# Kernel optimization log

Hardware: AMD Instinct MI355X
Metric: run time of the kernel (lower is better)

Reference implementation:

```python
import jax, jax.numpy as jnp
import numpy as np

F_TOKENS = 1024
D_TOKEN = 64
HIDDEN = 128


def setup_inputs() -> dict:
    key = jax.random.key(0)
    k1, k2, k3, k4, k5 = jax.random.split(key, 5)
    node = jax.random.normal(k1, (F_TOKENS, D_TOKEN), dtype=jnp.float32)
    # nn.Linear default init scale ~ 1/sqrt(fan_in); keep simple scaled randn
    W1 = jax.random.normal(k2, (2 * D_TOKEN, HIDDEN), dtype=jnp.float32) / np.sqrt(2 * D_TOKEN)
    b1 = jax.random.normal(k3, (HIDDEN,), dtype=jnp.float32) * 0.01
    w2 = jax.random.normal(k4, (HIDDEN,), dtype=jnp.float32) / np.sqrt(HIDDEN)
    b2 = jax.random.normal(k5, (1,), dtype=jnp.float32) * 0.01
    return {"node": node, "W1": W1, "b1": b1, "w2": w2, "b2": b2}


def reference(node, W1, b1, w2, b2):
    # Original: pair[i,j] = concat(node[i], node[j]);
    # Linear(2d->h) on the concat splits exactly into two d->h matmuls,
    # so we avoid materializing the [F,F,2d] concat tensor (same math).
    d = node.shape[1]
    a = node @ W1[:d]          # [F, h] contribution of v_i
    b = node @ W1[d:]          # [F, h] contribution of v_j
    h = jax.nn.gelu(a[:, None, :] + b[None, :, :] + b1, approximate=False)  # [F, F, h]
    logits = h @ w2 + b2[0]    # [F, F]
    return jax.nn.softmax(logits, axis=-1)
```

## Files before the change

kernel.cpp:

```cpp
#include <hip/hip_runtime.h>
#include <math.h>

#define F 1024
#define D 64
#define H 128

typedef float v2f __attribute__((ext_vector_type(2)));

__global__ __launch_bounds__(128) void prep_kernel(
    const float* __restrict__ node, const float* __restrict__ W1,
    const float* __restrict__ b1,
    float* __restrict__ A, float* __restrict__ Bt) {
  const int i = blockIdx.x;
  const int k = threadIdx.x;
  __shared__ float n[D];
  if (k < D) n[k] = node[i * D + k];
  __syncthreads();
  float a = b1[k];
  float b = 0.f;
#pragma unroll
  for (int r = 0; r < D; ++r) {
    const float nv = n[r];
    a = fmaf(nv, W1[r * H + k], a);
    b = fmaf(nv, W1[(D + r) * H + k], b);
  }
  A[i * H + k] = a;
  Bt[k * F + i] = b;
}

#define C1 (-2.3022082f)
#define C2 (-0.10294323f)

__device__ __forceinline__ void gelu_acc_pk(float a, v2f b, float wk, v2f& acc) {
  const v2f X = a + b;
  const v2f U = X * X;
  const v2f P = __builtin_elementwise_fma((v2f)(C2), U, (v2f)(C1));
  const v2f Arg = X * P;
  v2f E;
  E.x = __builtin_amdgcn_exp2f(Arg.x);
  E.y = __builtin_amdgcn_exp2f(Arg.y);
  const v2f Dn = 1.0f + E;
  v2f R;
  R.x = __builtin_amdgcn_rcpf(Dn.x);
  R.y = __builtin_amdgcn_rcpf(Dn.y);
  const v2f WX = wk * X;
  acc = __builtin_elementwise_fma(WX, R, acc);
}

__global__ __launch_bounds__(512) void pair_kernel(
    const float* __restrict__ A, const float* __restrict__ Bt,
    const float* __restrict__ w2, float* __restrict__ out) {
  const int i0 = blockIdx.x * 2;
  const int tid = threadIdx.x;

  __shared__ float4 sAW[H];
  __shared__ float redm[8][2];
  __shared__ float reds[8][2];

  if (tid < H)
    sAW[tid] = make_float4(A[i0 * H + tid], A[(i0 + 1) * H + tid], w2[tid], 0.f);
  __syncthreads();

  v2f acc0 = {0.f, 0.f};
  v2f acc1 = {0.f, 0.f};

  const v2f* bp = reinterpret_cast<const v2f*>(Bt) + tid;
#pragma unroll 8
  for (int k = 0; k < H; ++k) {
    const v2f b = *bp;
    bp += F / 2;
    const float4 aw = sAW[k];
    gelu_acc_pk(aw.x, b, aw.z, acc0);
    gelu_acc_pk(aw.y, b, aw.z, acc1);
  }

  const int wave = tid >> 6;
  const int lane = tid & 63;

  float m0 = fmaxf(acc0.x, acc0.y);
  float m1 = fmaxf(acc1.x, acc1.y);
#pragma unroll
  for (int off = 32; off >= 1; off >>= 1) {
    m0 = fmaxf(m0, __shfl_xor(m0, off, 64));
    m1 = fmaxf(m1, __shfl_xor(m1, off, 64));
  }
  if (lane == 0) {
    redm[wave][0] = m0;
    redm[wave][1] = m1;
  }
  __syncthreads();
  m0 = redm[0][0];
  m1 = redm[0][1];
#pragma unroll
  for (int w = 1; w < 8; ++w) {
    m0 = fmaxf(m0, redm[w][0]);
    m1 = fmaxf(m1, redm[w][1]);
  }

  float e00 = __expf(acc0.x - m0);
  float e01 = __expf(acc0.y - m0);
  float e10 = __expf(acc1.x - m1);
  float e11 = __expf(acc1.y - m1);
  float s0 = e00 + e01;
  float s1 = e10 + e11;
#pragma unroll
  for (int off = 32; off >= 1; off >>= 1) {
    s0 += __shfl_xor(s0, off, 64);
    s1 += __shfl_xor(s1, off, 64);
  }
  if (lane == 0) {
    reds[wave][0] = s0;
    reds[wave][1] = s1;
  }
  __syncthreads();
  s0 = 0.f;
  s1 = 0.f;
#pragma unroll
  for (int w = 0; w < 8; ++w) {
    s0 += reds[w][0];
    s1 += reds[w][1];
  }

  const float inv0 = __builtin_amdgcn_rcpf(s0);
  const float inv1 = __builtin_amdgcn_rcpf(s1);
  float2 o0, o1;
  o0.x = e00 * inv0;
  o0.y = e01 * inv0;
  o1.x = e10 * inv1;
  o1.y = e11 * inv1;
  *reinterpret_cast<float2*>(out + (size_t)i0 * F + 2 * tid) = o0;
  *reinterpret_cast<float2*>(out + (size_t)(i0 + 1) * F + 2 * tid) = o1;
}

extern "C" void kernel_launch(void* const* d_in, const int* in_sizes, int n_in,
                              void* d_out, int out_size, void* d_ws, size_t ws_size,
                              hipStream_t stream) {
  const float* node = (const float*)d_in[0];
  const float* W1   = (const float*)d_in[1];
  const float* b1   = (const float*)d_in[2];
  const float* w2   = (const float*)d_in[3];
  float* out = (float*)d_out;

  float* A  = (float*)d_ws;
  float* Bt = A + (size_t)F * H;

  prep_kernel<<<F, H, 0, stream>>>(node, W1, b1, A, Bt);
  pair_kernel<<<F / 2, 512, 0, stream>>>(A, Bt, w2, out);
}
```

Measured before the change: 44.34 us.

## Double-buffer Bt tiles into LDS via global_load_lds in pair kernel

Instead of each thread loading its Bt column pair directly from global memory on every k iteration, the pair kernel now stages 8-row tiles of Bt into shared memory with async global_load_lds, double-buffered. Compute on one tile overlaps the load of the next. The goal is to hide global-load latency behind the GELU arithmetic. In exchange it uses 64KB of LDS per block, which lowers occupancy, and it adds a barrier per tile. w2 is now read from global memory rather than packed into shared memory.

```diff
diff --git a/kernel.cpp b/kernel.cpp
--- a/kernel.cpp
+++ b/kernel.cpp
@@ -4,6 +4,8 @@
 #define F 1024
 #define D 64
 #define H 128
+#define BK 8
+#define NT (H / BK)
 
 typedef float v2f __attribute__((ext_vector_type(2)));
 
@@ -43,8 +45,7 @@
   v2f R;
   R.x = __builtin_amdgcn_rcpf(Dn.x);
   R.y = __builtin_amdgcn_rcpf(Dn.y);
-  const v2f WX = wk * X;
-  acc = __builtin_elementwise_fma(WX, R, acc);
+  acc = __builtin_elementwise_fma(wk * X, R, acc);
 }
 
 __global__ __launch_bounds__(512) void pair_kernel(
@@ -52,30 +53,61 @@
     const float* __restrict__ w2, float* __restrict__ out) {
   const int i0 = blockIdx.x * 2;
   const int tid = threadIdx.x;
+  const int wave = tid >> 6;
+  const int lane = tid & 63;
 
-  __shared__ float4 sAW[H];
+  __shared__ float bufs[2][BK * F];
+  __shared__ float2 sA[H];
   __shared__ float redm[8][2];
   __shared__ float reds[8][2];
 
   if (tid < H)
-    sAW[tid] = make_float4(A[i0 * H + tid], A[(i0 + 1) * H + tid], w2[tid], 0.f);
+    sA[tid] = make_float2(A[i0 * H + tid], A[(i0 + 1) * H + tid]);
+
+  const char* const bt_base = (const char*)Bt;
+#define STAGE(buf_, tile_)                                                   \
+  {                                                                          \
+    const char* src_ = bt_base + (size_t)(tile_) * (BK * F * 4);             \
+    _Pragma("unroll")                                                        \
+    for (int r_ = 0; r_ < 4; ++r_) {                                         \
+      const int chunk_ = r_ * 8192 + wave * 1024;                            \
+      __builtin_amdgcn_global_load_lds(                                      \
+          (const __attribute__((address_space(1))) void*)(src_ + chunk_ +    \
+                                                          lane * 16),        \
+          (__attribute__((address_space(3))) void*)((char*)&bufs[buf_][0] +  \
+                                                    chunk_),                 \
+          16, 0, 0);                                                         \
+    }                                                                        \
+  }
+
+  STAGE(0, 0);
   __syncthreads();
 
   v2f acc0 = {0.f, 0.f};
   v2f acc1 = {0.f, 0.f};
 
-  const v2f* bp = reinterpret_cast<const v2f*>(Bt) + tid;
-#pragma unroll 8
-  for (int k = 0; k < H; ++k) {
-    const v2f b = *bp;
-    bp += F / 2;
-    const float4 aw = sAW[k];
-    gelu_acc_pk(aw.x, b, aw.z, acc0);
-    gelu_acc_pk(aw.y, b, aw.z, acc1);
+#define COMPUTE(buf_, tile_)                                                 \
+  {                                                                          \
+    const float* bb_ = &bufs[buf_][2 * tid];                                 \
+    _Pragma("unroll")                                                        \
+    for (int kk_ = 0; kk_ < BK; ++kk_) {                                     \
+      const int k_ = (tile_)*BK + kk_;                                       \
+      const v2f b_ = *(const v2f*)(bb_ + kk_ * F);                           \
+      const float2 a2_ = sA[k_];                                             \
+      const float wk_ = w2[k_];                                              \
+      gelu_acc_pk(a2_.x, b_, wk_, acc0);                                     \
+      gelu_acc_pk(a2_.y, b_, wk_, acc1);                                     \
+    }                                                                        \
   }
 
-  const int wave = tid >> 6;
-  const int lane = tid & 63;
+  for (int t = 0; t < NT; t += 2) {
+    STAGE(1, t + 1);
+    COMPUTE(0, t);
+    __syncthreads();
+    if (t + 2 < NT) STAGE(0, t + 2);
+    COMPUTE(1, t + 1);
+    __syncthreads();
+  }
 
   float m0 = fmaxf(acc0.x, acc0.y);
   float m1 = fmaxf(acc1.x, acc1.y);
```

New measurement: 47.71 us. 1.08x slower.
